# Performance work log

Hardware: AMD Instinct MI355X
Metric: run time of the kernel (lower is better)

The kernel has to match this reference:

```python
import math
import jax, jax.numpy as jnp
import numpy as np

FACTOR = 2  # init kwarg `factor`

def setup_inputs() -> dict:
    key = jax.random.key(0)
    k1, k2, k3 = jax.random.split(key, 3)
    B, H, L, E = 32, 8, 2048, 64
    Q = jax.random.normal(k1, (B, H, L, E), dtype=jnp.float32)
    K = jax.random.normal(k2, (B, H, L, E), dtype=jnp.float32)
    V = jax.random.normal(k3, (B, H, L, E), dtype=jnp.float32)
    return {"Q": Q, "K": K, "V": V}

def _autocorrelation(Q, K, V):
    # Q, K, V: [B, H, L, E]; S == L so the pad/truncate branch is a no-op.
    B, H, L, E = Q.shape
    # FFT-based cross-correlation along the time axis (dim=2)
    q_fft = jnp.fft.rfft(Q, axis=2)
    k_fft = jnp.fft.rfft(K, axis=2)
    corr = jnp.fft.irfft(q_fft * jnp.conj(k_fft), n=L, axis=2)  # [B,H,L,E]
    # time_delay_agg
    top_k = int(FACTOR * math.log(L))  # = 15 for L=2048
    # torch.topk over dim=2 per (b,h,e): move L to last axis for lax.top_k
    weights, delays = jax.lax.top_k(jnp.swapaxes(corr, 2, 3), top_k)  # [B,H,E,k]
    weights = jax.nn.softmax(weights, axis=-1)
    # V.repeat(1,1,2,1) + gather(init+delay) is equivalent to a circular
    # gather from V with index (l + delay) mod L, since 0 <= init+delay <= 2L-2.
    base = jnp.arange(L)  # [L]
    out = jnp.zeros_like(V)
    for i in range(top_k):  # small fixed loop over top_k delays
        d_i = delays[..., i]                       # [B,H,E]
        idx = (base[None, None, :, None] + d_i[:, :, None, :]) % L  # [B,H,L,E]
        pattern = jnp.take_along_axis(V, idx, axis=2)               # [B,H,L,E]
        out = out + pattern * weights[..., i][:, :, None, :]
    return out

def reference(Q, K, V):
    return _autocorrelation(Q, K, V)
```

## Files before the change

kernel.cpp:

```cpp
#include <hip/hip_runtime.h>
#include <math.h>


#define LEN   2048
#define BH    256
#define NE    64
#define NSER  (BH * NE)
#define TOPK  15
#define NINF  (-INFINITY)

__device__ __forceinline__ int PC(int c) { return c + (c >> 4); }

__device__ __forceinline__ void sincos_tw(int idx, float& c, float& s) {
  float ang = (float)idx * (-6.283185307179586f / 2048.0f);
  __sincosf(ang, &s, &c);
}

template <bool INV>
__device__ __forceinline__ void dft8(float* xr, float* xi) {
  const float sg = INV ? -1.f : 1.f;
  const float c = 0.70710678118654752440f;
  float s0r = xr[0] + xr[4], s0i = xi[0] + xi[4];
  float s1r = xr[0] - xr[4], s1i = xi[0] - xi[4];
  float s2r = xr[2] + xr[6], s2i = xi[2] + xi[6];
  float s3r = xr[2] - xr[6], s3i = xi[2] - xi[6];
  float E0r = s0r + s2r, E0i = s0i + s2i;
  float E2r = s0r - s2r, E2i = s0i - s2i;
  float E1r = s1r + sg * s3i, E1i = s1i - sg * s3r;
  float E3r = s1r - sg * s3i, E3i = s1i + sg * s3r;
  float u0r = xr[1] + xr[5], u0i = xi[1] + xi[5];
  float u1r = xr[1] - xr[5], u1i = xi[1] - xi[5];
  float u2r = xr[3] + xr[7], u2i = xi[3] + xi[7];
  float u3r = xr[3] - xr[7], u3i = xi[3] - xi[7];
  float O0r = u0r + u2r, O0i = u0i + u2i;
  float O2r = u0r - u2r, O2i = u0i - u2i;
  float O1r = u1r + sg * u3i, O1i = u1i - sg * u3r;
  float O3r = u1r - sg * u3i, O3i = u1i + sg * u3r;
  float G0r = O0r, G0i = O0i;
  float G1r = O1r * c + O1i * (sg * c), G1i = O1i * c - O1r * (sg * c);
  float G2r = sg * O2i, G2i = -sg * O2r;
  float G3r = -O3r * c + O3i * (sg * c), G3i = -O3i * c - O3r * (sg * c);
  xr[0] = E0r + G0r; xi[0] = E0i + G0i;
  xr[1] = E1r + G1r; xi[1] = E1i + G1i;
  xr[2] = E2r + G2r; xi[2] = E2i + G2i;
  xr[3] = E3r + G3r; xi[3] = E3i + G3i;
  xr[4] = E0r - G0r; xi[4] = E0i - G0i;
  xr[5] = E1r - G1r; xi[5] = E1i - G1i;
  xr[6] = E2r - G2r; xi[6] = E2i - G2i;
  xr[7] = E3r - G3r; xi[7] = E3i - G3i;
}

template <bool INV>
__device__ __forceinline__ void dft4(float* xr, float* xi) {
  const float sg = INV ? -1.f : 1.f;
  float s0r = xr[0] + xr[2], s0i = xi[0] + xi[2];
  float s1r = xr[0] - xr[2], s1i = xi[0] - xi[2];
  float s2r = xr[1] + xr[3], s2i = xi[1] + xi[3];
  float s3r = xr[1] - xr[3], s3i = xi[1] - xi[3];
  xr[0] = s0r + s2r;        xi[0] = s0i + s2i;
  xr[1] = s1r + sg * s3i;   xi[1] = s1i - sg * s3r;
  xr[2] = s0r - s2r;        xi[2] = s0i - s2i;
  xr[3] = s1r - sg * s3i;   xi[3] = s1i + sg * s3r;
}

template <bool INV>
__device__ __forceinline__ void stage8_ip(float2* CB, int s, int sLog, int t) {
  float ar[8], ai[8];
#pragma unroll
  for (int r = 0; r < 8; ++r) {
    float2 v = CB[PC(t + 256 * r)];
    ar[r] = v.x; ai[r] = v.y;
  }
  __syncthreads();
  dft8<INV>(ar, ai);
  int q = t & (s - 1), p = t >> sLog;
  int ob = q + 8 * s * p;
  float c1, s1; sincos_tw(s * p, c1, s1);
  if (INV) s1 = -s1;
  CB[PC(ob)] = make_float2(ar[0], ai[0]);
  float wc = c1, wsn = s1;
#pragma unroll
  for (int j = 1; j < 8; ++j) {
    float zr = ar[j] * wc - ai[j] * wsn;
    float zi = ar[j] * wsn + ai[j] * wc;
    CB[PC(ob + s * j)] = make_float2(zr, zi);
    if (j < 7) {
      float nc = wc * c1 - wsn * s1;
      wsn = wc * s1 + wsn * c1;
      wc = nc;
    }
  }
  __syncthreads();
}


__global__ __launch_bounds__(256) void ktrans_qk(const float* __restrict__ Q,
                                                 const float* __restrict__ K,
                                                 float2* __restrict__ ZT) {
  int bh = blockIdx.x >> 5, l0 = (blockIdx.x & 31) * 64;
  __shared__ float sq[64][65], sk[64][65];
  int t = threadIdx.x;
  const float4* Qb = (const float4*)(Q + ((size_t)bh * LEN + l0) * NE);
  const float4* Kb = (const float4*)(K + ((size_t)bh * LEN + l0) * NE);
  int x = t & 15, c4 = x * 4;
#pragma unroll
  for (int it = 0; it < 4; ++it) {
    int row = (t >> 4) + it * 16;
    float4 q4 = Qb[row * 16 + x];
    float4 k4 = Kb[row * 16 + x];
    sq[row][c4 + 0] = q4.x; sq[row][c4 + 1] = q4.y;
    sq[row][c4 + 2] = q4.z; sq[row][c4 + 3] = q4.w;
    sk[row][c4 + 0] = k4.x; sk[row][c4 + 1] = k4.y;
    sk[row][c4 + 2] = k4.z; sk[row][c4 + 3] = k4.w;
  }
  __syncthreads();
  float2* Zb = ZT + (size_t)bh * NE * LEN + l0;
  int l2 = (t & 31) * 2;
#pragma unroll
  for (int it = 0; it < 8; ++it) {
    int e = (t >> 5) + it * 8;
    float4 o;
    o.x = sq[l2][e];     o.y = sk[l2][e];
    o.z = sq[l2 + 1][e]; o.w = sk[l2 + 1][e];
    *(float4*)&Zb[(size_t)e * LEN + l2] = o;
  }
}

__global__ __launch_bounds__(256) void ktrans_v(const float* __restrict__ src,
                                                float* __restrict__ dst) {
  int bh = blockIdx.x >> 5, l0 = (blockIdx.x & 31) * 64;
  __shared__ float sT[64][65];
  int t = threadIdx.x;
  const float4* Sb = (const float4*)(src + ((size_t)bh * LEN + l0) * NE);
  int x = t & 15, c4 = x * 4;
#pragma unroll
  for (int it = 0; it < 4; ++it) {
    int row = (t >> 4) + it * 16;
    float4 v4 = Sb[row * 16 + x];
    sT[row][c4 + 0] = v4.x; sT[row][c4 + 1] = v4.y;
    sT[row][c4 + 2] = v4.z; sT[row][c4 + 3] = v4.w;
  }
  __syncthreads();
  float* Db = dst + (size_t)bh * NE * LEN + l0;
  int l4 = x * 4;
#pragma unroll
  for (int it = 0; it < 4; ++it) {
    int e = (t >> 4) + it * 16;
    float4 o;
    o.x = sT[l4 + 0][e]; o.y = sT[l4 + 1][e];
    o.z = sT[l4 + 2][e]; o.w = sT[l4 + 3][e];
    *(float4*)&Db[(size_t)e * LEN + l4] = o;
  }
}


__global__ __launch_bounds__(256, 6) void kfft(const float2* __restrict__ ZT,
                                               float* __restrict__ Wt,
                                               int* __restrict__ Dl) {
  __shared__ float2 CB[2176];
  __shared__ float mv[64]; __shared__ int mi[64];
  const int t = threadIdx.x;
  const int wv = t >> 6, ln = t & 63;
  const float2* z = ZT + (size_t)blockIdx.x * LEN;

  {
    float ar[8], ai[8];
#pragma unroll
    for (int r = 0; r < 8; ++r) {
      float2 v = z[t + 256 * r];
      ar[r] = v.x; ai[r] = v.y;
    }
    dft8<false>(ar, ai);
    float c1, s1; sincos_tw(t, c1, s1);
    CB[PC(8 * t)] = make_float2(ar[0], ai[0]);
    float wc = c1, wsn = s1;
#pragma unroll
    for (int j = 1; j < 8; ++j) {
      float zr = ar[j] * wc - ai[j] * wsn;
      float zi = ar[j] * wsn + ai[j] * wc;
      CB[PC(8 * t + j)] = make_float2(zr, zi);
      if (j < 7) {
        float nc = wc * c1 - wsn * s1;
        wsn = wc * s1 + wsn * c1;
        wc = nc;
      }
    }
  }
  __syncthreads();
  stage8_ip<false>(CB, 8, 3, t);
  stage8_ip<false>(CB, 64, 6, t);
#pragma unroll
  for (int h = 0; h < 2; ++h) {
    int u = t + 256 * h;
    float xr[4], xi[4];
#pragma unroll
    for (int r = 0; r < 4; ++r) {
      float2 v = CB[PC(u + 512 * r)];
      xr[r] = v.x; xi[r] = v.y;
    }
    dft4<false>(xr, xi);
#pragma unroll
    for (int j = 0; j < 4; ++j) CB[PC(u + 512 * j)] = make_float2(xr[j], xi[j]);
  }
  __syncthreads();

  {
    float2 zf[4], zm[4];
#pragma unroll
    for (int r = 0; r < 4; ++r) {
      int f = t + 256 * r;
      int m = (LEN - f) & (LEN - 1);
      zf[r] = CB[PC(f)]; zm[r] = CB[PC(m)];
    }
    float2 e1 = make_float2(0.f, 0.f);
    if (t == 0) e1 = CB[PC(1024)];
    __syncthreads();
#pragma unroll
    for (int r = 0; r < 4; ++r) {
      int f = t + 256 * r;
      int m = (LEN - f) & (LEN - 1);
      float Xr = 0.5f * (zf[r].x + zm[r].x), Xi = 0.5f * (zf[r].y - zm[r].y);
      float Yr = 0.5f * (zf[r].y + zm[r].y), Yi = -0.5f * (zf[r].x - zm[r].x);
      CB[PC(f)] = make_float2(Xr * Yr + Xi * Yi, Xi * Yr - Xr * Yi);
      float Xr2 = 0.5f * (zm[r].x + zf[r].x), Xi2 = 0.5f * (zm[r].y - zf[r].y);
      float Yr2 = 0.5f * (zf[r].y + zm[r].y), Yi2 = -0.5f * (zm[r].x - zf[r].x);
      CB[PC(m)] = make_float2(Xr2 * Yr2 + Xi2 * Yi2, Xi2 * Yr2 - Xr2 * Yi2);
    }
    if (t == 0) CB[PC(1024)] = make_float2(e1.x * e1.y, 0.f);
  }
  __syncthreads();

  stage8_ip<true>(CB, 1, 0, t);
  stage8_ip<true>(CB, 8, 3, t);
  stage8_ip<true>(CB, 64, 6, t);
  float rv[8]; int ri[8];
#pragma unroll
  for (int h = 0; h < 2; ++h) {
    int u = t + 256 * h;
    float xr[4], xi[4];
#pragma unroll
    for (int r = 0; r < 4; ++r) {
      float2 v = CB[PC(u + 512 * r)];
      xr[r] = v.x; xi[r] = v.y;
    }
    dft4<true>(xr, xi);
#pragma unroll
    for (int j = 0; j < 4; ++j) {
      rv[h * 4 + j] = xr[j];
      ri[h * 4 + j] = u + 512 * j;
    }
  }

#define CE(i, j) { bool sw = rv[i] < rv[j];                                   \
    float tv = sw ? rv[j] : rv[i]; rv[j] = sw ? rv[i] : rv[j]; rv[i] = tv;    \
    int tx = sw ? ri[j] : ri[i];  ri[j] = sw ? ri[i] : ri[j];  ri[i] = tx; }
  CE(0,1) CE(2,3) CE(4,5) CE(6,7)
  CE(0,2) CE(1,3) CE(4,6) CE(5,7)
  CE(1,2) CE(5,6)
  CE(0,4) CE(1,5) CE(2,6) CE(3,7)
  CE(2,4) CE(3,5)
  CE(1,2) CE(3,4) CE(5,6)
#undef CE

  for (int it = 0; it < TOPK; ++it) {
    float bv = rv[0]; int bidx = ri[0];
#pragma unroll
    for (int off = 32; off >= 1; off >>= 1) {
      float ov = __shfl_xor(bv, off);
      int oi = __shfl_xor(bidx, off);
      bool btr = (ov > bv) || (ov == bv && oi < bidx);
      if (btr) { bv = ov; bidx = oi; }
    }
    if (ln == 0) { mv[wv * 16 + it] = bv; mi[wv * 16 + it] = bidx; }
    if (bidx == ri[0]) {
#pragma unroll
      for (int k = 0; k < 7; ++k) { rv[k] = rv[k + 1]; ri[k] = ri[k + 1]; }
      rv[7] = NINF;
    }
  }
  __syncthreads();

  if (wv == 0) {
    float v = ((ln & 15) < TOPK) ? mv[ln] : NINF;
    int ix = ((ln & 15) < TOPK) ? mi[ln] : 0;
    float myv = NINF; int myi = 0;
    for (int it = 0; it < TOPK; ++it) {
      float bv = v; int bidx = ix;
#pragma unroll
      for (int off = 32; off >= 1; off >>= 1) {
        float ov = __shfl_xor(bv, off);
        int oi = __shfl_xor(bidx, off);
        bool btr = (ov > bv) || (ov == bv && oi < bidx);
        if (btr) { bv = ov; bidx = oi; }
      }
      if (ln == it) { myv = bv; myi = bidx; }
      if (ix == bidx) v = NINF;
    }
    const float scl = 1.0f / 2048.0f;
    float vmax = __shfl(myv, 0);
    float e = (ln < TOPK) ? expf((myv - vmax) * scl) : 0.f;
    float ssum = e;
#pragma unroll
    for (int off = 1; off < 16; off <<= 1) ssum += __shfl_xor(ssum, off);
    if (ln < TOPK) {
      Wt[(size_t)blockIdx.x * 16 + ln] = e / ssum;
      Dl[(size_t)blockIdx.x * 16 + ln] = myi;
    }
  }
}


__global__ __launch_bounds__(256) void kgather_out(const float* __restrict__ VT,
                                                   const float* __restrict__ Wt,
                                                   const int* __restrict__ Dl,
                                                   float* __restrict__ out) {
  const int w = blockIdx.x;
  const int s = (w & 7) * 2048 + (w >> 3);
  const int bh = s >> 6, e = s & 63;
  __shared__ float v[LEN];
  const int t = threadIdx.x;
  const float4* src = (const float4*)(VT + (size_t)s * LEN);
  float4* vv = (float4*)v;
#pragma unroll
  for (int i = 0; i < 2; ++i) vv[t + 256 * i] = src[t + 256 * i];
  float wgt[TOPK]; int d[TOPK];
#pragma unroll
  for (int i = 0; i < TOPK; ++i) {
    wgt[i] = Wt[(size_t)s * 16 + i];
    d[i] = Dl[(size_t)s * 16 + i];
  }
  __syncthreads();
  float* dst = out + ((size_t)bh * LEN) * NE + e;
#pragma unroll
  for (int r = 0; r < 8; ++r) {
    int l = t + 256 * r;
    float acc = 0.f;
#pragma unroll
    for (int i = 0; i < TOPK; ++i) acc += wgt[i] * v[(l + d[i]) & (LEN - 1)];
    dst[(size_t)l * NE] = acc;
  }
}

extern "C" void kernel_launch(void* const* d_in, const int* in_sizes, int n_in,
                              void* d_out, int out_size, void* d_ws, size_t ws_size,
                              hipStream_t stream) {
  const float* Q = (const float*)d_in[0];
  const float* K = (const float*)d_in[1];
  const float* V = (const float*)d_in[2];
  float* out = (float*)d_out;
  char* ws = (char*)d_ws;

  const size_t ZT_BYTES = (size_t)NSER * LEN * sizeof(float2);
  float2* ZT = (float2*)ws;
  float* Wt = (float*)(ws + ZT_BYTES);
  int* Dl = (int*)(ws + ZT_BYTES + (size_t)NSER * 16 * sizeof(float));
  float* VT = (float*)ws;

  ktrans_qk<<<BH * 32, 256, 0, stream>>>(Q, K, ZT);
  kfft<<<NSER, 256, 0, stream>>>(ZT, Wt, Dl);
  ktrans_v<<<BH * 32, 256, 0, stream>>>(V, VT);
  kgather_out<<<NSER, 256, 0, stream>>>(VT, Wt, Dl, out);
}
```

Baseline: 859.0 us.

## Restructure gather to write coalesced output tiles and simplify top-k reductions

After: 919.6 us. +7.1%, slower.

```diff
diff --git a/kernel.cpp b/kernel.cpp
--- a/kernel.cpp
+++ b/kernel.cpp
@@ -12,8 +12,14 @@
 __device__ __forceinline__ int PC(int c) { return c + (c >> 4); }
 
 __device__ __forceinline__ void sincos_tw(int idx, float& c, float& s) {
+#if __has_builtin(__builtin_amdgcn_sinf) && __has_builtin(__builtin_amdgcn_cosf)
+  float rev = (float)idx * (-1.0f / 2048.0f);
+  s = __builtin_amdgcn_sinf(rev);
+  c = __builtin_amdgcn_cosf(rev);
+#else
   float ang = (float)idx * (-6.283185307179586f / 2048.0f);
   __sincosf(ang, &s, &c);
+#endif
 }
 
 template <bool INV>
@@ -154,9 +160,9 @@
 }
 
 
-__global__ __launch_bounds__(256, 6) void kfft(const float2* __restrict__ ZT,
-                                               float* __restrict__ Wt,
-                                               int* __restrict__ Dl) {
+__global__ __launch_bounds__(256) void kfft(const float2* __restrict__ ZT,
+                                            float* __restrict__ Wt,
+                                            int* __restrict__ Dl) {
   __shared__ float2 CB[2176];
   __shared__ float mv[64]; __shared__ int mi[64];
   const int t = threadIdx.x;
@@ -263,16 +269,15 @@
 #undef CE
 
   for (int it = 0; it < TOPK; ++it) {
-    float bv = rv[0]; int bidx = ri[0];
-#pragma unroll
-    for (int off = 32; off >= 1; off >>= 1) {
-      float ov = __shfl_xor(bv, off);
-      int oi = __shfl_xor(bidx, off);
-      bool btr = (ov > bv) || (ov == bv && oi < bidx);
-      if (btr) { bv = ov; bidx = oi; }
-    }
-    if (ln == 0) { mv[wv * 16 + it] = bv; mi[wv * 16 + it] = bidx; }
-    if (bidx == ri[0]) {
+    float bv = rv[0];
+#pragma unroll
+    for (int off = 32; off >= 1; off >>= 1)
+      bv = fmaxf(bv, __shfl_xor(bv, off));
+    unsigned long long m = __ballot(rv[0] == bv);
+    int winlane = __ffsll(m) - 1;
+    int widx = __shfl(ri[0], winlane);
+    if (ln == 0) { mv[wv * 16 + it] = bv; mi[wv * 16 + it] = widx; }
+    if (ln == winlane) {
 #pragma unroll
       for (int k = 0; k < 7; ++k) { rv[k] = rv[k + 1]; ri[k] = ri[k + 1]; }
       rv[7] = NINF;
@@ -285,16 +290,15 @@
     int ix = ((ln & 15) < TOPK) ? mi[ln] : 0;
     float myv = NINF; int myi = 0;
     for (int it = 0; it < TOPK; ++it) {
-      float bv = v; int bidx = ix;
-#pragma unroll
-      for (int off = 32; off >= 1; off >>= 1) {
-        float ov = __shfl_xor(bv, off);
-        int oi = __shfl_xor(bidx, off);
-        bool btr = (ov > bv) || (ov == bv && oi < bidx);
-        if (btr) { bv = ov; bidx = oi; }
-      }
-      if (ln == it) { myv = bv; myi = bidx; }
-      if (ix == bidx) v = NINF;
+      float bv = v;
+#pragma unroll
+      for (int off = 32; off >= 1; off >>= 1)
+        bv = fmaxf(bv, __shfl_xor(bv, off));
+      unsigned long long m = __ballot(v == bv);
+      int winlane = __ffsll(m) - 1;
+      int widx = __shfl(ix, winlane);
+      if (ln == it) { myv = bv; myi = widx; }
+      if (ln == winlane) v = NINF;
     }
     const float scl = 1.0f / 2048.0f;
     float vmax = __shfl(myv, 0);
@@ -310,34 +314,56 @@
 }
 
 
-__global__ __launch_bounds__(256) void kgather_out(const float* __restrict__ VT,
-                                                   const float* __restrict__ Wt,
-                                                   const int* __restrict__ Dl,
-                                                   float* __restrict__ out) {
-  const int w = blockIdx.x;
-  const int s = (w & 7) * 2048 + (w >> 3);
-  const int bh = s >> 6, e = s & 63;
-  __shared__ float v[LEN];
+__global__ __launch_bounds__(256) void kgather_bh(const float* __restrict__ VT,
+                                                  const float* __restrict__ Wt,
+                                                  const int* __restrict__ Dl,
+                                                  float* __restrict__ out) {
+  int d = blockIdx.x;
+  int x = d & 7, k = d >> 3;
+  int bh = x * 32 + (k >> 3);
+  int ls = k & 7;
   const int t = threadIdx.x;
-  const float4* src = (const float4*)(VT + (size_t)s * LEN);
-  float4* vv = (float4*)v;
-#pragma unroll
-  for (int i = 0; i < 2; ++i) vv[t + 256 * i] = src[t + 256 * i];
-  float wgt[TOPK]; int d[TOPK];
-#pragma unroll
-  for (int i = 0; i < TOPK; ++i) {
-    wgt[i] = Wt[(size_t)s * 16 + i];
-    d[i] = Dl[(size_t)s * 16 + i];
-  }
-  __syncthreads();
-  float* dst = out + ((size_t)bh * LEN) * NE + e;
-#pragma unroll
-  for (int r = 0; r < 8; ++r) {
-    int l = t + 256 * r;
-    float acc = 0.f;
-#pragma unroll
-    for (int i = 0; i < TOPK; ++i) acc += wgt[i] * v[(l + d[i]) & (LEN - 1)];
-    dst[(size_t)l * NE] = acc;
+  const int wv = t >> 6, ln = t & 63;
+
+  __shared__ float lw[64][16];
+  __shared__ int   ldl[64][16];
+  __shared__ float tile[64][65];
+
+  const float* Wb = Wt + (size_t)bh * NE * 16;
+  const int*   Db = Dl + (size_t)bh * NE * 16;
+#pragma unroll
+  for (int i = 0; i < 4; ++i) {
+    int idx = t + i * 256;
+    lw[idx >> 4][idx & 15] = Wb[idx];
+    ldl[idx >> 4][idx & 15] = Db[idx];
+  }
+  __syncthreads();
+
+  const float* Vbh = VT + (size_t)bh * NE * LEN;
+  for (int lt = 0; lt < 4; ++lt) {
+    int l0 = ls * 256 + lt * 64;
+    for (int ei = 0; ei < 16; ++ei) {
+      int e = ei * 4 + wv;
+      const float* vrow = Vbh + (size_t)e * LEN;
+      float acc = 0.f;
+#pragma unroll
+      for (int i = 0; i < TOPK; ++i) {
+        int dd = ldl[e][i];
+        float ww = lw[e][i];
+        acc += ww * vrow[(l0 + ln + dd) & (LEN - 1)];
+      }
+      tile[ln][e] = acc;
+    }
+    __syncthreads();
+    int r = t >> 2, c0 = (t & 3) * 16;
+    float* orow = out + ((size_t)bh * LEN + l0 + r) * NE + c0;
+#pragma unroll
+    for (int j = 0; j < 4; ++j) {
+      float4 o = make_float4(tile[r][c0 + 4 * j + 0], tile[r][c0 + 4 * j + 1],
+                             tile[r][c0 + 4 * j + 2], tile[r][c0 + 4 * j + 3]);
+      ((float4*)orow)[j] = o;
+    }
+    __syncthreads();
   }
 }
 
@@ -359,5 +385,5 @@
   ktrans_qk<<<BH * 32, 256, 0, stream>>>(Q, K, ZT);
   kfft<<<NSER, 256, 0, stream>>>(ZT, Wt, Dl);
   ktrans_v<<<BH * 32, 256, 0, stream>>>(V, VT);
-  kgather_out<<<NSER, 256, 0, stream>>>(VT, Wt, Dl, out);
-}
+  kgather_bh<<<BH * 8, 256, 0, stream>>>(VT, Wt, Dl, out);
+}
```
